# Optimization experiments

Measured on AMD Instinct MI355X. Metric: run time of the kernel, lower is better.

## Reference

```python
import jax, jax.numpy as jnp
import numpy as np

OUT_H, OUT_W, STRIDE = 100, 100, 4  # hardcoded in the torch module


def _downsample(pc):
    # pc: (B, 3, H, W) -> permute to (B, H, W, 3), strided-subsample, flatten to (B, N, 3)
    pc = jnp.transpose(pc, (0, 2, 3, 1))
    pc = pc[:, : OUT_H * STRIDE : STRIDE, : OUT_W * STRIDE : STRIDE, :]
    return pc.reshape(pc.shape[0], OUT_H * OUT_W, 3)


def setup_inputs() -> dict:
    key = jax.random.key(0)
    k1, k2 = jax.random.split(key)
    B, H, W = 4, 400, 400
    return {
        "target_pc": jax.random.normal(k1, (B, 3, H, W), dtype=jnp.float32),
        "source_pc": jax.random.normal(k2, (B, 3, H, W), dtype=jnp.float32),
    }


def reference(target_pc, source_pc):
    t = _downsample(target_pc)  # (B, N, 3) query points
    s = _downsample(source_pc)  # (B, N, 3) reference points
    # Squared Euclidean distances (B, Nt, Ns); argmin is identical for L2 vs L2^2.
    d2 = (
        jnp.sum(t * t, axis=-1)[:, :, None]
        + jnp.sum(s * s, axis=-1)[:, None, :]
        - 2.0 * jnp.einsum("bnd,bmd->bnm", t, s)
    )
    idx = jnp.argmin(d2, axis=-1)  # (B, Nt): nearest source index for each target point
    nearest = jnp.take_along_axis(s, idx[..., None], axis=1)  # (B, Nt, 3)
    per_batch = jnp.mean((nearest - t) ** 2, axis=(1, 2))  # MSE per batch element
    return jnp.mean(per_batch)
```

## Files before the change

### kernel.cpp

```cpp
#include <hip/hip_runtime.h>


#define BATCH  4
#define NPTS   10000
#define NPAD   10240
#define H      400
#define W      400
#define STRIDE 4
#define OUTW   100
#define NC     32
#define CHUNK  313
#define CPAD   316
#define BLOCK  256
#define TPT    4
#define TBLKS  10
#define RBLOCK 256

__device__ __forceinline__ float min3f(float a, float b, float c) {
    float r;
    asm("v_min3_f32 %0, %1, %2, %3" : "=v"(r) : "v"(a), "v"(b), "v"(c));
    return r;
}

__global__ void prep_kernel(const float* __restrict__ tgt,
                            const float* __restrict__ src,
                            float4* __restrict__ S4,
                            float4* __restrict__ T4) {
    int gid = blockIdx.x * blockDim.x + threadIdx.x;
    if (gid < BATCH * NPAD) {
        int b = gid / NPAD;
        int n = gid % NPAD;
        float4 v = make_float4(0.f, 0.f, 0.f, 0.f);
        if (n < NPTS) {
            int h = n / OUTW, w = n % OUTW;
            int base = ((b * 3) * H + h * STRIDE) * W + w * STRIDE;
            float x = tgt[base];
            float y = tgt[base + H * W];
            float z = tgt[base + 2 * H * W];
            v = make_float4(x, y, z, x * x + y * y + z * z);
        }
        T4[gid] = v;
    } else {
        int sid = gid - BATCH * NPAD;
        if (sid < BATCH * NPTS) {
            int b = sid / NPTS;
            int m = sid % NPTS;
            int h = m / OUTW, w = m % OUTW;
            int base = ((b * 3) * H + h * STRIDE) * W + w * STRIDE;
            float x = src[base];
            float y = src[base + H * W];
            float z = src[base + 2 * H * W];
            S4[sid] = make_float4(-2.f * x, -2.f * y, -2.f * z,
                                  x * x + y * y + z * z);
        }
    }
}

#define COMPUTE4(q0, q1, q2, q3)                                   \
    _Pragma("unroll")                                              \
    for (int k = 0; k < TPT; k++) {                                \
        float d0 = fmaf(tx[k], q0.x, q0.w);                        \
        d0 = fmaf(ty[k], q0.y, d0);                                \
        d0 = fmaf(tz[k], q0.z, d0);                                \
        float d1 = fmaf(tx[k], q1.x, q1.w);                        \
        d1 = fmaf(ty[k], q1.y, d1);                                \
        d1 = fmaf(tz[k], q1.z, d1);                                \
        float d2 = fmaf(tx[k], q2.x, q2.w);                        \
        d2 = fmaf(ty[k], q2.y, d2);                                \
        d2 = fmaf(tz[k], q2.z, d2);                                \
        float d3 = fmaf(tx[k], q3.x, q3.w);                        \
        d3 = fmaf(ty[k], q3.y, d3);                                \
        d3 = fmaf(tz[k], q3.z, d3);                                \
        mn[k] = min3f(mn[k], min3f(d0, d1, d2), d3);               \
    }

__global__ __launch_bounds__(BLOCK) void knn_kernel(
        const float4* __restrict__ S4,
        const float4* __restrict__ T4,
        float* __restrict__ M2) {
    __shared__ float4 lds[CPAD];
    const int tblk = blockIdx.x;
    const int cblk = blockIdx.y;
    const int b    = blockIdx.z;
    const int tid  = threadIdx.x;

    const int s0    = cblk * CHUNK;
    const int valid = (NPTS - s0 < CHUNK) ? (NPTS - s0) : CHUNK;
    const float4* sbase = S4 + b * NPTS + s0;
    for (int i = tid; i < CPAD; i += BLOCK)
        lds[i] = (i < valid) ? sbase[i] : make_float4(0.f, 0.f, 0.f, 3.0e38f);

    const int tbase = b * NPAD + tblk * (BLOCK * TPT) + tid;
    float tx[TPT], ty[TPT], tz[TPT], mn[TPT];
#pragma unroll
    for (int k = 0; k < TPT; k++) {
        float4 t = T4[tbase + k * BLOCK];
        tx[k] = t.x; ty[k] = t.y; tz[k] = t.z;
        mn[k] = 3.0e38f;
    }
    __syncthreads();

    float4 c0 = lds[0], c1 = lds[1], c2 = lds[2], c3 = lds[3];
    for (int j = 4; j < CPAD; j += 4) {
        float4 n0 = lds[j + 0];
        float4 n1 = lds[j + 1];
        float4 n2 = lds[j + 2];
        float4 n3 = lds[j + 3];
        COMPUTE4(c0, c1, c2, c3)
        c0 = n0; c1 = n1; c2 = n2; c3 = n3;
    }
    COMPUTE4(c0, c1, c2, c3)

    float* obase = M2 + (cblk * BATCH + b) * NPAD + tblk * (BLOCK * TPT) + tid;
#pragma unroll
    for (int k = 0; k < TPT; k++) obase[k * BLOCK] = mn[k];
}

__global__ void reduce_kernel(const float* __restrict__ M2,
                              const float4* __restrict__ T4,
                              float* __restrict__ out) {
    __shared__ float red[RBLOCK / 64];
    int gid = blockIdx.x * RBLOCK + threadIdx.x;
    float val = 0.f;
    if (gid < BATCH * NPTS) {
        int b = gid / NPTS;
        int n = gid % NPTS;
        float m = 3.0e38f;
#pragma unroll
        for (int c = 0; c < NC; c++)
            m = fminf(m, M2[(c * BATCH + b) * NPAD + n]);
        float tt = T4[b * NPAD + n].w;
        val = fmaxf(m + tt, 0.f);
    }
#pragma unroll
    for (int off = 32; off > 0; off >>= 1)
        val += __shfl_down(val, off, 64);
    int lane = threadIdx.x & 63;
    int wave = threadIdx.x >> 6;
    if (lane == 0) red[wave] = val;
    __syncthreads();
    if (threadIdx.x == 0) {
        float s = 0.f;
        for (int wv = 0; wv < RBLOCK / 64; wv++) s += red[wv];
        atomicAdd(out, s * (1.0f / (BATCH * NPTS * 3)));
    }
}

extern "C" void kernel_launch(void* const* d_in, const int* in_sizes, int n_in,
                              void* d_out, int out_size, void* d_ws, size_t ws_size,
                              hipStream_t stream) {
    const float* tgt = (const float*)d_in[0];
    const float* src = (const float*)d_in[1];
    float* out = (float*)d_out;

    char* ws = (char*)d_ws;
    float4* S4 = (float4*)ws;
    float4* T4 = (float4*)(ws + (size_t)BATCH * NPTS * 16);
    float*  M2 = (float*)(ws + (size_t)BATCH * NPTS * 16
                             + (size_t)BATCH * NPAD * 16);

    hipMemsetAsync(out, 0, sizeof(float), stream);

    int nprep = BATCH * NPAD + BATCH * NPTS;
    prep_kernel<<<(nprep + RBLOCK - 1) / RBLOCK, RBLOCK, 0, stream>>>(tgt, src, S4, T4);

    knn_kernel<<<dim3(TBLKS, NC, BATCH), BLOCK, 0, stream>>>(S4, T4, M2);

    reduce_kernel<<<(BATCH * NPTS + RBLOCK - 1) / RBLOCK, RBLOCK, 0, stream>>>(
        M2, T4, out);
}
```

Measured before the change: 104.9 us.

## Use packed FP32 FMA with SoA shared-memory layout in KNN inner loop

Splits the source chunk in shared memory from AoS float4 into separate x/y/z/w arrays and evaluates two candidate distances per instruction with v_pk_fma_f32, with target coordinates broadcast into 2-wide vectors. The aim is to roughly halve the VALU instruction count of the distance loop, which is the main cost. CPAD grows to 320 so the loop processes two float4 groups per iteration. In exchange, target values now occupy twice the registers, and the packed FMA may not issue at twice the scalar rate.

```diff
diff --git a/kernel.cpp b/kernel.cpp
--- a/kernel.cpp
+++ b/kernel.cpp
@@ -10,16 +10,24 @@
 #define OUTW   100
 #define NC     32
 #define CHUNK  313
-#define CPAD   316
+#define CPAD   320
 #define BLOCK  256
 #define TPT    4
 #define TBLKS  10
 #define RBLOCK 256
 
+typedef float float2v __attribute__((ext_vector_type(2)));
+
 __device__ __forceinline__ float min3f(float a, float b, float c) {
     float r;
     asm("v_min3_f32 %0, %1, %2, %3" : "=v"(r) : "v"(a), "v"(b), "v"(c));
     return r;
+}
+
+__device__ __forceinline__ float2v pk_fma(float2v a, float2v b, float2v c) {
+    float2v d;
+    asm("v_pk_fma_f32 %0, %1, %2, %3" : "=v"(d) : "v"(a), "v"(b), "v"(c));
+    return d;
 }
 
 __global__ void prep_kernel(const float* __restrict__ tgt,
@@ -56,29 +64,25 @@
     }
 }
 
-#define COMPUTE4(q0, q1, q2, q3)                                   \
-    _Pragma("unroll")                                              \
-    for (int k = 0; k < TPT; k++) {                                \
-        float d0 = fmaf(tx[k], q0.x, q0.w);                        \
-        d0 = fmaf(ty[k], q0.y, d0);                                \
-        d0 = fmaf(tz[k], q0.z, d0);                                \
-        float d1 = fmaf(tx[k], q1.x, q1.w);                        \
-        d1 = fmaf(ty[k], q1.y, d1);                                \
-        d1 = fmaf(tz[k], q1.z, d1);                                \
-        float d2 = fmaf(tx[k], q2.x, q2.w);                        \
-        d2 = fmaf(ty[k], q2.y, d2);                                \
-        d2 = fmaf(tz[k], q2.z, d2);                                \
-        float d3 = fmaf(tx[k], q3.x, q3.w);                        \
-        d3 = fmaf(ty[k], q3.y, d3);                                \
-        d3 = fmaf(tz[k], q3.z, d3);                                \
-        mn[k] = min3f(mn[k], min3f(d0, d1, d2), d3);               \
+#define COMPUTE_GROUP(qx, qy, qz, qw)                                       \
+    _Pragma("unroll")                                                       \
+    for (int k = 0; k < TPT; k++) {                                         \
+        float2v d01 = pk_fma((float2v){qx.x, qx.y}, txp[k],                 \
+                             (float2v){qw.x, qw.y});                        \
+        d01 = pk_fma((float2v){qy.x, qy.y}, typ[k], d01);                   \
+        d01 = pk_fma((float2v){qz.x, qz.y}, tzp[k], d01);                   \
+        float2v d23 = pk_fma((float2v){qx.z, qx.w}, txp[k],                 \
+                             (float2v){qw.z, qw.w});                        \
+        d23 = pk_fma((float2v){qy.z, qy.w}, typ[k], d23);                   \
+        d23 = pk_fma((float2v){qz.z, qz.w}, tzp[k], d23);                   \
+        mn[k] = min3f(mn[k], min3f(d01.x, d01.y, d23.x), d23.y);            \
     }
 
 __global__ __launch_bounds__(BLOCK) void knn_kernel(
         const float4* __restrict__ S4,
         const float4* __restrict__ T4,
         float* __restrict__ M2) {
-    __shared__ float4 lds[CPAD];
+    __shared__ float4 SX[CPAD / 4], SY[CPAD / 4], SZ[CPAD / 4], SW[CPAD / 4];
     const int tblk = blockIdx.x;
     const int cblk = blockIdx.y;
     const int b    = blockIdx.z;
@@ -87,29 +91,34 @@
     const int s0    = cblk * CHUNK;
     const int valid = (NPTS - s0 < CHUNK) ? (NPTS - s0) : CHUNK;
     const float4* sbase = S4 + b * NPTS + s0;
-    for (int i = tid; i < CPAD; i += BLOCK)
-        lds[i] = (i < valid) ? sbase[i] : make_float4(0.f, 0.f, 0.f, 3.0e38f);
+    for (int i = tid; i < CPAD; i += BLOCK) {
+        float4 s = (i < valid) ? sbase[i]
+                               : make_float4(0.f, 0.f, 0.f, 3.0e38f);
+        ((float*)SX)[i] = s.x;
+        ((float*)SY)[i] = s.y;
+        ((float*)SZ)[i] = s.z;
+        ((float*)SW)[i] = s.w;
+    }
 
     const int tbase = b * NPAD + tblk * (BLOCK * TPT) + tid;
-    float tx[TPT], ty[TPT], tz[TPT], mn[TPT];
+    float2v txp[TPT], typ[TPT], tzp[TPT];
+    float mn[TPT];
 #pragma unroll
     for (int k = 0; k < TPT; k++) {
         float4 t = T4[tbase + k * BLOCK];
-        tx[k] = t.x; ty[k] = t.y; tz[k] = t.z;
+        txp[k] = (float2v){t.x, t.x};
+        typ[k] = (float2v){t.y, t.y};
+        tzp[k] = (float2v){t.z, t.z};
         mn[k] = 3.0e38f;
     }
     __syncthreads();
 
-    float4 c0 = lds[0], c1 = lds[1], c2 = lds[2], c3 = lds[3];
-    for (int j = 4; j < CPAD; j += 4) {
-        float4 n0 = lds[j + 0];
-        float4 n1 = lds[j + 1];
-        float4 n2 = lds[j + 2];
-        float4 n3 = lds[j + 3];
-        COMPUTE4(c0, c1, c2, c3)
-        c0 = n0; c1 = n1; c2 = n2; c3 = n3;
+    for (int g = 0; g < CPAD / 4; g += 2) {
+        float4 ax = SX[g],     ay = SY[g],     az = SZ[g],     aw = SW[g];
+        float4 bx = SX[g + 1], by = SY[g + 1], bz = SZ[g + 1], bw = SW[g + 1];
+        COMPUTE_GROUP(ax, ay, az, aw)
+        COMPUTE_GROUP(bx, by, bz, bw)
     }
-    COMPUTE4(c0, c1, c2, c3)
 
     float* obase = M2 + (cblk * BATCH + b) * NPAD + tblk * (BLOCK * TPT) + tid;
 #pragma unroll
```

New measurement: 99.77 us. -4.9%, faster.
